# Optimization experiments

Measured on AMD Instinct MI355X. Metric: run time of the kernel, lower is better.

The kernel has to match this reference:

```python
import jax, jax.numpy as jnp
import numpy as np

B, S, D, H, F = 4, 2048, 512, 8, 2048
HD = D // H
SCALE = HD ** -0.5


def layernorm(x, g, b, eps=1e-5):
    mu = jnp.mean(x, axis=-1, keepdims=True)
    var = jnp.var(x, axis=-1, keepdims=True)
    return (x - mu) * jax.lax.rsqrt(var + eps) * g + b


def setup_inputs() -> dict:
    key = jax.random.key(0)
    ks = jax.random.split(key, 10)
    s = 0.02
    return {
        "x": jax.random.normal(ks[0], (B, S, D), jnp.float32),
        "w_qkv": jax.random.normal(ks[1], (D, 3 * D), jnp.float32) * s,
        "b_qkv": jnp.zeros((3 * D,), jnp.float32),
        "w_o": jax.random.normal(ks[2], (D, D), jnp.float32) * s,
        "b_o": jnp.zeros((D,), jnp.float32),
        "w1": jax.random.normal(ks[3], (D, F), jnp.float32) * s,
        "b1": jnp.zeros((F,), jnp.float32),
        "w2": jax.random.normal(ks[4], (F, D), jnp.float32) * s,
        "b2": jnp.zeros((D,), jnp.float32),
        "g1": jnp.ones((D,), jnp.float32),
        "be1": jnp.zeros((D,), jnp.float32),
        "g2": jnp.ones((D,), jnp.float32),
        "be2": jnp.zeros((D,), jnp.float32),
    }


def reference(x, w_qkv, b_qkv, w_o, b_o, w1, b1, w2, b2, g1, be1, g2, be2):
    res = x
    qkv = x @ w_qkv + b_qkv                       # [B,S,3D]
    q, k, v = jnp.split(qkv, 3, axis=-1)          # each [B,S,D]
    # head partition: [B,S,D] -> [B,H,S,hd]
    def split_heads(t):
        return t.reshape(B, S, H, HD).transpose(0, 2, 1, 3)
    q, k, v = map(split_heads, (q, k, v))
    scores = jnp.einsum('bhqc,bhkc->bhqk', q, k) * SCALE
    weights = jax.nn.softmax(scores, axis=-1)
    out = jnp.einsum('bhqk,bhkc->bhqc', weights, v)
    out = out.transpose(0, 2, 1, 3).reshape(B, S, D)  # merge heads
    out = out @ w_o + b_o
    out = layernorm(out + res, g1, be1)
    res = out
    out = jax.nn.gelu(out @ w1 + b1, approximate=False) @ w2 + b2
    out = layernorm(out + res, g2, be2)
    return out
```

## Files before the change

### kernel.cpp

```cpp
#include <hip/hip_runtime.h>
#include <math.h>

constexpr int B = 4, S = 2048, D = 512, H = 8, HD = 64, F = 2048;
constexpr int M = B * S;
constexpr float C_QK = 0.125f * 1.44269504088896340736f;

typedef __bf16 bf16x8 __attribute__((ext_vector_type(8)));
typedef float  f32x4  __attribute__((ext_vector_type(4)));
typedef float  f32x16 __attribute__((ext_vector_type(16)));

static __device__ __forceinline__ short f2bf(float f) {
  return __builtin_bit_cast(short, (__bf16)f);
}

static __device__ __forceinline__ void gload16(const void* g, void* l) {
  __builtin_amdgcn_global_load_lds(
      (const __attribute__((address_space(1))) unsigned int*)g,
      (__attribute__((address_space(3))) unsigned int*)l, 16, 0, 0);
}

__global__ __launch_bounds__(256)
void prep_all(const float* __restrict__ x, short* __restrict__ xb,
              const float* __restrict__ w_qkv, short* __restrict__ wtq,
              const float* __restrict__ w_o,  short* __restrict__ wto,
              const float* __restrict__ w1,   short* __restrict__ wt1,
              const float* __restrict__ w2,   short* __restrict__ wt2) {
  __shared__ float tl[32][33];
  const int id = blockIdx.x;
  const int t = threadIdx.x;
  if (id < 4096) {
    int i = id * 256 + t;
    float4 v = ((const float4*)x)[i];
    ((short4*)xb)[i] = make_short4(f2bf(v.x), f2bf(v.y), f2bf(v.z), f2bf(v.w));
    return;
  }
  const float* in; short* out; int R, C, bx, by;
  if (id < 4864)      { int k = id - 4096; in = w_qkv; out = wtq; R = 512;  C = 1536; bx = k % 48; by = k / 48; }
  else if (id < 5120) { int k = id - 4864; in = w_o;   out = wto; R = 512;  C = 512;  bx = k % 16; by = k / 16; }
  else if (id < 6144) { int k = id - 5120; in = w1;    out = wt1; R = 512;  C = 2048; bx = k % 64; by = k / 64; }
  else                { int k = id - 6144; in = w2;    out = wt2; R = 2048; C = 512;  bx = k % 16; by = k / 16; }
  const int r0 = by * 32, c0 = bx * 32;
  const int tr = t >> 3, tc4 = (t & 7) * 4;
  float4 v = *(const float4*)&in[(size_t)(r0 + tr) * C + c0 + tc4];
  tl[tr][tc4] = v.x; tl[tr][tc4 + 1] = v.y; tl[tr][tc4 + 2] = v.z; tl[tr][tc4 + 3] = v.w;
  __syncthreads();
  short4 o = make_short4(f2bf(tl[tc4][tr]), f2bf(tl[tc4 + 1][tr]),
                         f2bf(tl[tc4 + 2][tr]), f2bf(tl[tc4 + 3][tr]));
  *(short4*)&out[(size_t)(c0 + tr) * R + r0 + tc4] = o;
}

template<int BM, int BN, int GELU, int EPI>
__global__ __launch_bounds__(256)
void gemm_bf16(const short* __restrict__ A, const short* __restrict__ Wt,
               const float* __restrict__ bias,
               float* __restrict__ Cf, short* __restrict__ Cb,
               short* __restrict__ qsw, short* __restrict__ ksw,
               short* __restrict__ vsw, int K, int N) {
  constexpr int MI = BM / 32, NI = BN / 32;
  __shared__ short As[2][BM * 64] __attribute__((aligned(16)));
  __shared__ short Bs[2][BN * 64] __attribute__((aligned(16)));
  const int t = threadIdx.x;
  const int w = t >> 6, l = t & 63, g = l >> 4, r = l & 15;
  const int wm = w >> 1, wn = w & 1;
  const int m0 = blockIdx.y * BM, n0 = blockIdx.x * BN;

  auto stage = [&](int buf, int k0) {
#pragma unroll
    for (int i = 0; i < BM / 32; ++i) {
      int q = i * 256 + t;
      int row = q >> 3, sl = (q & 7) ^ (row & 7);
      gload16(A + (size_t)(m0 + row) * K + k0 + sl * 8, (char*)As[buf] + q * 16);
    }
#pragma unroll
    for (int i = 0; i < BN / 32; ++i) {
      int q = i * 256 + t;
      int row = q >> 3, sl = (q & 7) ^ (row & 7);
      gload16(Wt + (size_t)(n0 + row) * K + k0 + sl * 8, (char*)Bs[buf] + q * 16);
    }
  };

  f32x4 acc[MI][NI] = {};
  const int NS = K >> 6;
  stage(0, 0);
  __syncthreads();
  for (int st = 0; st < NS; ++st) {
    const int cur = st & 1;
    if (st + 1 < NS) stage(cur ^ 1, (st + 1) << 6);
    const short* Ac = As[cur];
    const short* Bc = Bs[cur];
#pragma unroll
    for (int kh = 0; kh < 2; ++kh) {
      const int cc = kh * 4 + g;
      bf16x8 aF[MI], bF[NI];
#pragma unroll
      for (int mi = 0; mi < MI; ++mi) {
        const int row = wm * (MI * 16) + mi * 16 + r;
        aF[mi] = *(const bf16x8*)(Ac + row * 64 + ((cc ^ (r & 7)) << 3));
      }
#pragma unroll
      for (int ni = 0; ni < NI; ++ni) {
        const int row = wn * (NI * 16) + ni * 16 + r;
        bF[ni] = *(const bf16x8*)(Bc + row * 64 + ((cc ^ (r & 7)) << 3));
      }
#pragma unroll
      for (int mi = 0; mi < MI; ++mi)
#pragma unroll
        for (int ni = 0; ni < NI; ++ni)
          acc[mi][ni] = __builtin_amdgcn_mfma_f32_16x16x32_bf16(aF[mi], bF[ni], acc[mi][ni], 0, 0, 0);
    }
    __syncthreads();
  }

#pragma unroll
  for (int mi = 0; mi < MI; ++mi) {
#pragma unroll
    for (int ni = 0; ni < NI; ++ni) {
      const int n  = n0 + wn * (NI * 16) + ni * 16 + r;
      const int mB = m0 + wm * (MI * 16) + mi * 16 + g * 4;
      float vals[4];
#pragma unroll
      for (int j = 0; j < 4; ++j) {
        float v = acc[mi][ni][j] + bias[n];
        if (GELU) v = 0.5f * v * (1.0f + erff(v * 0.70710678118654752f));
        vals[j] = v;
      }
      if (EPI == 0) {
#pragma unroll
        for (int j = 0; j < 4; ++j) Cf[(size_t)(mB + j) * N + n] = vals[j];
      } else if (EPI == 1) {
#pragma unroll
        for (int j = 0; j < 4; ++j) Cb[(size_t)(mB + j) * N + n] = f2bf(vals[j]);
      } else {
        const int b = mB >> 11, s = mB & 2047;
        if (n < 512) {
          const int hh = n >> 6, d = n & 63;
          const size_t rb = (size_t)(b * 8 + hh) * 2048;
#pragma unroll
          for (int j = 0; j < 4; ++j)
            qsw[(rb + s + j) * 64 + (d ^ (((s + j) & 7) << 3))] = f2bf(vals[j] * C_QK);
        } else if (n < 1024) {
          const int hh = (n - 512) >> 6, d = (n - 512) & 63;
          const size_t rb = (size_t)(b * 8 + hh) * 2048;
#pragma unroll
          for (int j = 0; j < 4; ++j)
            ksw[(rb + s + j) * 64 + (d ^ (((s + j) & 7) << 3))] = f2bf(vals[j]);
        } else {
          const int hh = (n - 1024) >> 6, d = (n - 1024) & 63;
          short4 pk = make_short4(f2bf(vals[0]), f2bf(vals[1]), f2bf(vals[2]), f2bf(vals[3]));
          *(short4*)&vsw[(size_t)((b * 8 + hh) * 64 + d) * 2048 + (s ^ ((d & 7) << 3))] = pk;
        }
      }
    }
  }
}

__global__ __launch_bounds__(256)
void attn_mfma(const short* __restrict__ qsw, const short* __restrict__ ksw,
               const short* __restrict__ vsw, short* __restrict__ Opart,
               float* __restrict__ Lpart) {
  __shared__ short Ks[2][64 * 64] __attribute__((aligned(16)));
  __shared__ short Vs[2][64 * 64] __attribute__((aligned(16)));
  const int t = threadIdx.x;
  const int w = t >> 6, l = t & 63;
  const int c = l & 31, hi = l >> 5;
  const int bh = blockIdx.y;
  const int q0 = blockIdx.x * 128;
  const int half = blockIdx.z;
  const int kbase = half * 1024;
  const short* qb = qsw + ((size_t)bh * 2048 + q0) * 64;
  const short* kb = ksw + (size_t)bh * 2048 * 64;
  const short* vb = vsw + (size_t)bh * 64 * 2048;

  auto stage_kv = [&](int buf, int kt) {
#pragma unroll
    for (int i = 0; i < 2; ++i) {
      int q = i * 256 + t;
      gload16(kb + (size_t)(kt + (q >> 3)) * 64 + (q & 7) * 8, (char*)Ks[buf] + q * 16);
    }
#pragma unroll
    for (int i = 0; i < 2; ++i) {
      int q = i * 256 + t;
      gload16(vb + (size_t)(q >> 3) * 2048 + kt + (q & 7) * 8, (char*)Vs[buf] + q * 16);
    }
  };

  const int qrow = w * 32 + c;
  const int swz = (c & 7) << 3;
  bf16x8 qf[4];
#pragma unroll
  for (int dc = 0; dc < 4; ++dc)
    qf[dc] = *(const bf16x8*)(qb + qrow * 64 + ((dc * 16 + hi * 8) ^ swz));

  stage_kv(0, kbase);
  __syncthreads();

  f32x16 o0 = {}, o1 = {};
  float m_run = -3e38f, l_run = 0.0f;

  for (int ti = 0; ti < 16; ++ti) {
    const int cur = ti & 1;
    if (ti < 15) stage_kv(cur ^ 1, kbase + (ti + 1) * 64);
    const short* Kc = Ks[cur];
    const short* Vc = Vs[cur];

    f32x16 s0 = {}, s1 = {};
    __builtin_amdgcn_s_setprio(1);
#pragma unroll
    for (int dc = 0; dc < 4; ++dc) {
      const int koff = (dc * 16 + hi * 8) ^ swz;
      bf16x8 kf0 = *(const bf16x8*)(Kc + c * 64 + koff);
      bf16x8 kf1 = *(const bf16x8*)(Kc + (32 + c) * 64 + koff);
      s0 = __builtin_amdgcn_mfma_f32_32x32x16_bf16(kf0, qf[dc], s0, 0, 0, 0);
      s1 = __builtin_amdgcn_mfma_f32_32x32x16_bf16(kf1, qf[dc], s1, 0, 0, 0);
    }
    __builtin_amdgcn_s_setprio(0);

    float tmax = -3e38f;
#pragma unroll
    for (int j = 0; j < 16; ++j) tmax = fmaxf(tmax, fmaxf(s0[j], s1[j]));
    tmax = fmaxf(tmax, __shfl_xor(tmax, 32, 64));
    if (__any(tmax - m_run > 8.0f)) {
      float mnew = fmaxf(m_run, tmax);
      float rs = __builtin_amdgcn_exp2f(m_run - mnew);
      m_run = mnew;
      l_run *= rs;
#pragma unroll
      for (int j = 0; j < 16; ++j) {
        float rj = __shfl(rs, (j & 3) + 8 * (j >> 2) + 4 * hi, 64);
        o0[j] *= rj; o1[j] *= rj;
      }
    }
    float rsum = 0.0f;
#pragma unroll
    for (int j = 0; j < 16; ++j) {
      s0[j] = __builtin_amdgcn_exp2f(s0[j] - m_run);
      s1[j] = __builtin_amdgcn_exp2f(s1[j] - m_run);
      rsum += s0[j] + s1[j];
    }
    rsum += __shfl_xor(rsum, 32, 64);
    l_run += rsum;

    __builtin_amdgcn_s_setprio(1);
#pragma unroll
    for (int kc = 0; kc < 4; ++kc) {
      const int jb = (kc & 1) * 8;
      int u0, u1, v0, v1;
      if (kc < 2) {
        asm("v_cvt_pk_bf16_f32 %0, %1, %2" : "=v"(u0) : "v"(s0[jb + 0]), "v"(s0[jb + 1]));
        asm("v_cvt_pk_bf16_f32 %0, %1, %2" : "=v"(u1) : "v"(s0[jb + 2]), "v"(s0[jb + 3]));
        asm("v_cvt_pk_bf16_f32 %0, %1, %2" : "=v"(v0) : "v"(s0[jb + 4]), "v"(s0[jb + 5]));
        asm("v_cvt_pk_bf16_f32 %0, %1, %2" : "=v"(v1) : "v"(s0[jb + 6]), "v"(s0[jb + 7]));
      } else {
        asm("v_cvt_pk_bf16_f32 %0, %1, %2" : "=v"(u0) : "v"(s1[jb + 0]), "v"(s1[jb + 1]));
        asm("v_cvt_pk_bf16_f32 %0, %1, %2" : "=v"(u1) : "v"(s1[jb + 2]), "v"(s1[jb + 3]));
        asm("v_cvt_pk_bf16_f32 %0, %1, %2" : "=v"(v0) : "v"(s1[jb + 4]), "v"(s1[jb + 5]));
        asm("v_cvt_pk_bf16_f32 %0, %1, %2" : "=v"(v1) : "v"(s1[jb + 6]), "v"(s1[jb + 7]));
      }
      asm volatile("v_permlane32_swap_b32 %0, %1" : "+v"(u0), "+v"(v0));
      asm volatile("v_permlane32_swap_b32 %0, %1" : "+v"(u1), "+v"(v1));
      int pw[4] = {u0, u1, v0, v1};
      bf16x8 pa = __builtin_bit_cast(bf16x8, *(int4*)pw);
      const int voff = (kc * 16 + hi * 8) ^ swz;
      bf16x8 vf0 = *(const bf16x8*)(Vc + c * 64 + voff);
      bf16x8 vf1 = *(const bf16x8*)(Vc + (32 + c) * 64 + voff);
      o0 = __builtin_amdgcn_mfma_f32_32x32x16_bf16(pa, vf0, o0, 0, 0, 0);
      o1 = __builtin_amdgcn_mfma_f32_32x32x16_bf16(pa, vf1, o1, 0, 0, 0);
    }
    __builtin_amdgcn_s_setprio(0);
    __syncthreads();
  }

  const size_t hrow = (size_t)half * (32 * 2048) + (size_t)bh * 2048;
  float inv = 1.0f / l_run;
  if (hi == 0)
    Lpart[hrow + q0 + w * 32 + c] = m_run + __builtin_log2f(l_run);
#pragma unroll
  for (int j = 0; j < 16; ++j) {
    const int q_rel = (j & 3) + 8 * (j >> 2) + 4 * hi;
    float invq = __shfl(inv, q_rel, 64);
    const size_t row = (hrow + q0 + w * 32 + q_rel) * 64;
    Opart[row + c]      = f2bf(o0[j] * invq);
    Opart[row + 32 + c] = f2bf(o1[j] * invq);
  }
}

__global__ __launch_bounds__(256)
void attn_combine(const short* __restrict__ Opart, const float* __restrict__ Lpart,
                  short* __restrict__ a_o) {
  const int idx = blockIdx.x * 256 + threadIdx.x;
  const int row = idx >> 3;
  const int d8 = (idx & 7) * 8;
  const float L0 = Lpart[row], L1 = Lpart[65536 + row];
  const float mx = fmaxf(L0, L1);
  const float w0 = __builtin_amdgcn_exp2f(L0 - mx), w1 = __builtin_amdgcn_exp2f(L1 - mx);
  const float inv = 1.0f / (w0 + w1);
  bf16x8 a = *(const bf16x8*)(Opart + (size_t)row * 64 + d8);
  bf16x8 b = *(const bf16x8*)(Opart + ((size_t)65536 + row) * 64 + d8);
  bf16x8 res;
#pragma unroll
  for (int i = 0; i < 8; ++i)
    res[i] = (__bf16)((w0 * (float)a[i] + w1 * (float)b[i]) * inv);
  const int bh = row >> 11, s = row & 2047;
  const int bb = bh >> 3, hh = bh & 7;
  *(bf16x8*)(a_o + ((size_t)(bb * 2048 + s)) * 512 + hh * 64 + d8) = res;
}

template<int WB>
__global__ __launch_bounds__(256)
void add_ln(const float* __restrict__ a, const float* __restrict__ res,
            const float* __restrict__ g_, const float* __restrict__ be,
            float* __restrict__ out, short* __restrict__ outb) {
  const int row = blockIdx.x;
  const int t = threadIdx.x;
  const size_t off = (size_t)row * D;
  float x0 = a[off + t] + res[off + t];
  float x1 = a[off + t + 256] + res[off + t + 256];
  float sum = x0 + x1;
  float sq  = x0 * x0 + x1 * x1;
#pragma unroll
  for (int o2 = 32; o2 > 0; o2 >>= 1) {
    sum += __shfl_down(sum, o2);
    sq  += __shfl_down(sq, o2);
  }
  __shared__ float ssum[4], ssq[4];
  const int wid = t >> 6;
  if ((t & 63) == 0) { ssum[wid] = sum; ssq[wid] = sq; }
  __syncthreads();
  if (t == 0) {
    ssum[0] = ssum[0] + ssum[1] + ssum[2] + ssum[3];
    ssq[0]  = ssq[0] + ssq[1] + ssq[2] + ssq[3];
  }
  __syncthreads();
  float mu   = ssum[0] * (1.0f / D);
  float var  = ssq[0] * (1.0f / D) - mu * mu;
  float rstd = rsqrtf(var + 1e-5f);
  float y0 = (x0 - mu) * rstd * g_[t] + be[t];
  float y1 = (x1 - mu) * rstd * g_[t + 256] + be[t + 256];
  out[off + t] = y0;
  out[off + t + 256] = y1;
  if (WB) {
    outb[off + t] = f2bf(y0);
    outb[off + t + 256] = f2bf(y1);
  }
}

extern "C" void kernel_launch(void* const* d_in, const int* in_sizes, int n_in,
                              void* d_out, int out_size, void* d_ws, size_t ws_size,
                              hipStream_t stream) {
  const float* x     = (const float*)d_in[0];
  const float* w_qkv = (const float*)d_in[1];
  const float* b_qkv = (const float*)d_in[2];
  const float* w_o   = (const float*)d_in[3];
  const float* b_o   = (const float*)d_in[4];
  const float* w1    = (const float*)d_in[5];
  const float* b1    = (const float*)d_in[6];
  const float* w2    = (const float*)d_in[7];
  const float* b2    = (const float*)d_in[8];
  const float* g1    = (const float*)d_in[9];
  const float* be1   = (const float*)d_in[10];
  const float* g2    = (const float*)d_in[11];
  const float* be2   = (const float*)d_in[12];
  float* out = (float*)d_out;
  (void)in_sizes; (void)n_in; (void)out_size; (void)ws_size;

  const size_t MD = (size_t)M * 512;
  short* q_sw = (short*)d_ws;
  short* k_sw = q_sw + MD;
  short* v_sw = k_sw + MD;
  short* a_o  = v_sw + MD;
  short* h    = q_sw;
  short* xb   = a_o + MD;
  short* ln1b = xb;
  short* wtq  = xb + MD;
  short* wto  = wtq + (size_t)1536 * 512;
  short* wt1  = wto + (size_t)512 * 512;
  short* wt2  = wt1 + (size_t)512 * 2048;
  float* buf  = (float*)(wt2 + (size_t)2048 * 512);
  float* ln1  = buf + MD;
  short* Opart = (short*)(ln1 + MD);
  float* Lpart = (float*)(Opart + (size_t)2 * 32 * 2048 * 64);

  prep_all<<<7168, 256, 0, stream>>>(x, xb, w_qkv, wtq, w_o, wto, w1, wt1, w2, wt2);

  gemm_bf16<128, 64, 0, 2><<<dim3(24, 64), 256, 0, stream>>>(
      xb, wtq, b_qkv, nullptr, nullptr, q_sw, k_sw, v_sw, 512, 1536);
  attn_mfma<<<dim3(16, 32, 2), 256, 0, stream>>>(q_sw, k_sw, v_sw, Opart, Lpart);
  attn_combine<<<2048, 256, 0, stream>>>(Opart, Lpart, a_o);
  gemm_bf16<64, 64, 0, 0><<<dim3(8, 128), 256, 0, stream>>>(
      a_o, wto, b_o, buf, nullptr, nullptr, nullptr, nullptr, 512, 512);
  add_ln<1><<<M, 256, 0, stream>>>(buf, x, g1, be1, ln1, ln1b);
  gemm_bf16<128, 64, 1, 1><<<dim3(32, 64), 256, 0, stream>>>(
      ln1b, wt1, b1, nullptr, h, nullptr, nullptr, nullptr, 512, 2048);
  gemm_bf16<64, 64, 0, 0><<<dim3(8, 128), 256, 0, stream>>>(
      h, wt2, b2, buf, nullptr, nullptr, nullptr, nullptr, 2048, 512);
  add_ln<0><<<M, 256, 0, stream>>>(buf, ln1, g2, be2, out, nullptr);
}
```

Before: 295.1 us.

## Single-buffer KV tiles and process score halves sequentially to raise occupancy

New measurement: 285.1 us. 1.04x faster.

```diff
diff --git a/kernel.cpp b/kernel.cpp
--- a/kernel.cpp
+++ b/kernel.cpp
@@ -154,36 +154,22 @@
   }
 }
 
-__global__ __launch_bounds__(256)
+__global__ __launch_bounds__(256, 4)
 void attn_mfma(const short* __restrict__ qsw, const short* __restrict__ ksw,
                const short* __restrict__ vsw, short* __restrict__ Opart,
                float* __restrict__ Lpart) {
-  __shared__ short Ks[2][64 * 64] __attribute__((aligned(16)));
-  __shared__ short Vs[2][64 * 64] __attribute__((aligned(16)));
+  __shared__ short Ks[64 * 64] __attribute__((aligned(16)));
+  __shared__ short Vs[64 * 64] __attribute__((aligned(16)));
   const int t = threadIdx.x;
   const int w = t >> 6, l = t & 63;
   const int c = l & 31, hi = l >> 5;
   const int bh = blockIdx.y;
   const int q0 = blockIdx.x * 128;
-  const int half = blockIdx.z;
-  const int kbase = half * 1024;
+  const int kbase = blockIdx.z * 1024;
   const short* qb = qsw + ((size_t)bh * 2048 + q0) * 64;
   const short* kb = ksw + (size_t)bh * 2048 * 64;
   const short* vb = vsw + (size_t)bh * 64 * 2048;
 
-  auto stage_kv = [&](int buf, int kt) {
-#pragma unroll
-    for (int i = 0; i < 2; ++i) {
-      int q = i * 256 + t;
-      gload16(kb + (size_t)(kt + (q >> 3)) * 64 + (q & 7) * 8, (char*)Ks[buf] + q * 16);
-    }
-#pragma unroll
-    for (int i = 0; i < 2; ++i) {
-      int q = i * 256 + t;
-      gload16(vb + (size_t)(q >> 3) * 2048 + kt + (q & 7) * 8, (char*)Vs[buf] + q * 16);
-    }
-  };
-
   const int qrow = w * 32 + c;
   const int swz = (c & 7) << 3;
   bf16x8 qf[4];
@@ -191,86 +177,84 @@
   for (int dc = 0; dc < 4; ++dc)
     qf[dc] = *(const bf16x8*)(qb + qrow * 64 + ((dc * 16 + hi * 8) ^ swz));
 
-  stage_kv(0, kbase);
-  __syncthreads();
-
   f32x16 o0 = {}, o1 = {};
   float m_run = -3e38f, l_run = 0.0f;
 
   for (int ti = 0; ti < 16; ++ti) {
-    const int cur = ti & 1;
-    if (ti < 15) stage_kv(cur ^ 1, kbase + (ti + 1) * 64);
-    const short* Kc = Ks[cur];
-    const short* Vc = Vs[cur];
-
-    f32x16 s0 = {}, s1 = {};
-    __builtin_amdgcn_s_setprio(1);
-#pragma unroll
-    for (int dc = 0; dc < 4; ++dc) {
-      const int koff = (dc * 16 + hi * 8) ^ swz;
-      bf16x8 kf0 = *(const bf16x8*)(Kc + c * 64 + koff);
-      bf16x8 kf1 = *(const bf16x8*)(Kc + (32 + c) * 64 + koff);
-      s0 = __builtin_amdgcn_mfma_f32_32x32x16_bf16(kf0, qf[dc], s0, 0, 0, 0);
-      s1 = __builtin_amdgcn_mfma_f32_32x32x16_bf16(kf1, qf[dc], s1, 0, 0, 0);
-    }
-    __builtin_amdgcn_s_setprio(0);
-
-    float tmax = -3e38f;
-#pragma unroll
-    for (int j = 0; j < 16; ++j) tmax = fmaxf(tmax, fmaxf(s0[j], s1[j]));
-    tmax = fmaxf(tmax, __shfl_xor(tmax, 32, 64));
-    if (__any(tmax - m_run > 8.0f)) {
-      float mnew = fmaxf(m_run, tmax);
-      float rs = __builtin_amdgcn_exp2f(m_run - mnew);
-      m_run = mnew;
-      l_run *= rs;
+    const int kt = kbase + ti * 64;
+    __syncthreads();
+#pragma unroll
+    for (int i = 0; i < 2; ++i) {
+      int q = i * 256 + t;
+      gload16(kb + (size_t)(kt + (q >> 3)) * 64 + (q & 7) * 8, (char*)Ks + q * 16);
+    }
+#pragma unroll
+    for (int i = 0; i < 2; ++i) {
+      int q = i * 256 + t;
+      gload16(vb + (size_t)(q >> 3) * 2048 + kt + (q & 7) * 8, (char*)Vs + q * 16);
+    }
+    __syncthreads();
+
+#pragma unroll
+    for (int h2 = 0; h2 < 2; ++h2) {
+      f32x16 s = {};
+      __builtin_amdgcn_s_setprio(1);
+#pragma unroll
+      for (int dc = 0; dc < 4; ++dc) {
+        const int koff = (dc * 16 + hi * 8) ^ swz;
+        bf16x8 kf = *(const bf16x8*)(Ks + (h2 * 32 + c) * 64 + koff);
+        s = __builtin_amdgcn_mfma_f32_32x32x16_bf16(kf, qf[dc], s, 0, 0, 0);
+      }
+      __builtin_amdgcn_s_setprio(0);
+
+      float tmax = -3e38f;
+#pragma unroll
+      for (int j = 0; j < 16; ++j) tmax = fmaxf(tmax, s[j]);
+      tmax = fmaxf(tmax, __shfl_xor(tmax, 32, 64));
+      if (__any(tmax - m_run > 8.0f)) {
+        float mnew = fmaxf(m_run, tmax);
+        float rs = __builtin_amdgcn_exp2f(m_run - mnew);
+        m_run = mnew;
+        l_run *= rs;
+#pragma unroll
+        for (int j = 0; j < 16; ++j) {
+          float rj = __shfl(rs, (j & 3) + 8 * (j >> 2) + 4 * hi, 64);
+          o0[j] *= rj; o1[j] *= rj;
+        }
+      }
+      float rsum = 0.0f;
 #pragma unroll
       for (int j = 0; j < 16; ++j) {
-        float rj = __shfl(rs, (j & 3) + 8 * (j >> 2) + 4 * hi, 64);
-        o0[j] *= rj; o1[j] *= rj;
-      }
-    }
-    float rsum = 0.0f;
-#pragma unroll
-    for (int j = 0; j < 16; ++j) {
-      s0[j] = __builtin_amdgcn_exp2f(s0[j] - m_run);
-      s1[j] = __builtin_amdgcn_exp2f(s1[j] - m_run);
-      rsum += s0[j] + s1[j];
-    }
-    rsum += __shfl_xor(rsum, 32, 64);
-    l_run += rsum;
-
-    __builtin_amdgcn_s_setprio(1);
-#pragma unroll
-    for (int kc = 0; kc < 4; ++kc) {
-      const int jb = (kc & 1) * 8;
-      int u0, u1, v0, v1;
-      if (kc < 2) {
-        asm("v_cvt_pk_bf16_f32 %0, %1, %2" : "=v"(u0) : "v"(s0[jb + 0]), "v"(s0[jb + 1]));
-        asm("v_cvt_pk_bf16_f32 %0, %1, %2" : "=v"(u1) : "v"(s0[jb + 2]), "v"(s0[jb + 3]));
-        asm("v_cvt_pk_bf16_f32 %0, %1, %2" : "=v"(v0) : "v"(s0[jb + 4]), "v"(s0[jb + 5]));
-        asm("v_cvt_pk_bf16_f32 %0, %1, %2" : "=v"(v1) : "v"(s0[jb + 6]), "v"(s0[jb + 7]));
-      } else {
-        asm("v_cvt_pk_bf16_f32 %0, %1, %2" : "=v"(u0) : "v"(s1[jb + 0]), "v"(s1[jb + 1]));
-        asm("v_cvt_pk_bf16_f32 %0, %1, %2" : "=v"(u1) : "v"(s1[jb + 2]), "v"(s1[jb + 3]));
-        asm("v_cvt_pk_bf16_f32 %0, %1, %2" : "=v"(v0) : "v"(s1[jb + 4]), "v"(s1[jb + 5]));
-        asm("v_cvt_pk_bf16_f32 %0, %1, %2" : "=v"(v1) : "v"(s1[jb + 6]), "v"(s1[jb + 7]));
-      }
-      asm volatile("v_permlane32_swap_b32 %0, %1" : "+v"(u0), "+v"(v0));
-      asm volatile("v_permlane32_swap_b32 %0, %1" : "+v"(u1), "+v"(v1));
-      int pw[4] = {u0, u1, v0, v1};
-      bf16x8 pa = __builtin_bit_cast(bf16x8, *(int4*)pw);
-      const int voff = (kc * 16 + hi * 8) ^ swz;
-      bf16x8 vf0 = *(const bf16x8*)(Vc + c * 64 + voff);
-      bf16x8 vf1 = *(const bf16x8*)(Vc + (32 + c) * 64 + voff);
-      o0 = __builtin_amdgcn_mfma_f32_32x32x16_bf16(pa, vf0, o0, 0, 0, 0);
-      o1 = __builtin_amdgcn_mfma_f32_32x32x16_bf16(pa, vf1, o1, 0, 0, 0);
-    }
-    __builtin_amdgcn_s_setprio(0);
-    __syncthreads();
-  }
-
-  const size_t hrow = (size_t)half * (32 * 2048) + (size_t)bh * 2048;
+        s[j] = __builtin_amdgcn_exp2f(s[j] - m_run);
+        rsum += s[j];
+      }
+      rsum += __shfl_xor(rsum, 32, 64);
+      l_run += rsum;
+
+      __builtin_amdgcn_s_setprio(1);
+#pragma unroll
+      for (int kc = 0; kc < 2; ++kc) {
+        const int jb = kc * 8;
+        int u0, u1, v0, v1;
+        asm("v_cvt_pk_bf16_f32 %0, %1, %2" : "=v"(u0) : "v"(s[jb + 0]), "v"(s[jb + 1]));
+        asm("v_cvt_pk_bf16_f32 %0, %1, %2" : "=v"(u1) : "v"(s[jb + 2]), "v"(s[jb + 3]));
+        asm("v_cvt_pk_bf16_f32 %0, %1, %2" : "=v"(v0) : "v"(s[jb + 4]), "v"(s[jb + 5]));
+        asm("v_cvt_pk_bf16_f32 %0, %1, %2" : "=v"(v1) : "v"(s[jb + 6]), "v"(s[jb + 7]));
+        asm volatile("v_permlane32_swap_b32 %0, %1" : "+v"(u0), "+v"(v0));
+        asm volatile("v_permlane32_swap_b32 %0, %1" : "+v"(u1), "+v"(v1));
+        int pw[4] = {u0, u1, v0, v1};
+        bf16x8 pa = __builtin_bit_cast(bf16x8, *(int4*)pw);
+        const int voff = ((h2 * 32 + kc * 16 + hi * 8)) ^ swz;
+        bf16x8 vf0 = *(const bf16x8*)(Vs + c * 64 + voff);
+        bf16x8 vf1 = *(const bf16x8*)(Vs + (32 + c) * 64 + voff);
+        o0 = __builtin_amdgcn_mfma_f32_32x32x16_bf16(pa, vf0, o0, 0, 0, 0);
+        o1 = __builtin_amdgcn_mfma_f32_32x32x16_bf16(pa, vf1, o1, 0, 0, 0);
+      }
+      __builtin_amdgcn_s_setprio(0);
+    }
+  }
+
+  const size_t hrow = (size_t)blockIdx.z * (32 * 2048) + (size_t)bh * 2048;
   float inv = 1.0f / l_run;
   if (hi == 0)
     Lpart[hrow + q0 + w * 32 + c] = m_run + __builtin_log2f(l_run);
```
